# Performance work log

Hardware: AMD Instinct MI355X
Metric: run time of the kernel (lower is better)

Reference implementation:

```python
import jax, jax.numpy as jnp
import numpy as np

B, S, D = 2, 2048, 1024
H, HKV, DK = 16, 4, 64          # n_heads, n_kv_heads, head dim
NREP = H // HKV                  # 4


def apply_rope(x):
    # Faithful to the original: positions run over x.shape[-2], which is the
    # HEAD axis (x is [B, S, H, DK]) due to how the torch module is written.
    d = x.shape[-1]
    h = x.shape[-2]
    inv_freq = 1.0 / (10000.0 ** (jnp.arange(0, d, 2, dtype=jnp.float32) / d))
    freqs = jnp.arange(h, dtype=jnp.float32)[:, None] * inv_freq[None, :]  # [H, DK/2]
    cos, sin = jnp.cos(freqs), jnp.sin(freqs)
    x1, x2 = x[..., 0::2], x[..., 1::2]
    # interleave back: stack on new last axis then flatten
    return jnp.stack([x1 * cos - x2 * sin, x1 * sin + x2 * cos], axis=-1).reshape(x.shape)


def setup_inputs() -> dict:
    key = jax.random.key(0)
    kx, kq, kk, kv, ko = jax.random.split(key, 5)
    std = 0.02
    x = jax.random.normal(kx, (B, S, D), jnp.float32)
    w_q = jax.random.normal(kq, (D, H * DK), jnp.float32) * std
    w_k = jax.random.normal(kk, (D, HKV * DK), jnp.float32) * std
    w_v = jax.random.normal(kv, (D, HKV * DK), jnp.float32) * std
    w_o = jax.random.normal(ko, (D, D), jnp.float32) * std
    # causal mask, broadcastable to [B, H, S, S]
    mask = jnp.tril(jnp.ones((S, S), bool))[None, None]  # [1,1,S,S]
    return {"x": x, "w_q": w_q, "w_k": w_k, "w_v": w_v, "w_o": w_o, "mask": mask}


def reference(x, w_q, w_k, w_v, w_o, mask):
    b, s, d = x.shape
    Q = (x @ w_q).reshape(b, s, H, DK)
    K = (x @ w_k).reshape(b, s, HKV, DK)
    V = (x @ w_v).reshape(b, s, HKV, DK)
    Q = apply_rope(Q)
    K = apply_rope(K)
    # [B,H,S,DK] with query heads grouped per kv head (matches repeat_interleave)
    Q = Q.transpose(0, 2, 1, 3).reshape(b, HKV, NREP, s, DK)
    K = K.transpose(0, 2, 1, 3)  # [B,HKV,S,DK]
    V = V.transpose(0, 2, 1, 3)
    scores = jnp.einsum('bgrqd,bgkd->bgrqk', Q, K) / np.float32(np.sqrt(DK))
    scores = scores.astype(jnp.float32)
    neg = jnp.finfo(jnp.float32).min
    scores = jnp.where(mask[:, :, None, :, :], scores, neg)  # [1,1,1,S,S] broadcast
    w = jax.nn.softmax(scores, axis=-1)
    ctx = jnp.einsum('bgrqk,bgkd->bgrqd', w, V)  # [B,HKV,NREP,S,DK]
    ctx = ctx.reshape(b, H, s, DK).transpose(0, 2, 1, 3).reshape(b, s, d)
    return ctx @ w_o
```

## Files before the change

### kernel.cpp

```cpp
#include <hip/hip_runtime.h>
#include <hip/hip_bf16.h>

#define S_LEN 2048
#define NBATCH 2
#define DMODEL 1024
#define NHEAD 16
#define NKV 4
#define HDIM 64

typedef __attribute__((ext_vector_type(4))) float f32x4;
typedef __attribute__((ext_vector_type(8))) short s16x8;

#define QSCALE 0.18033688011112042f

__device__ __forceinline__ unsigned short f32_bf16(float f) {
    unsigned int u = __float_as_uint(f);
    u += 0x7FFFu + ((u >> 16) & 1u);
    return (unsigned short)(u >> 16);
}

__global__ __launch_bounds__(256) void cvt_bf16_k(const float* __restrict__ in,
                                                  unsigned short* __restrict__ out, int n4) {
    int i = blockIdx.x * 256 + threadIdx.x;
    if (i < n4) {
        const float4 v = reinterpret_cast<const float4*>(in)[i];
        ushort4 r;
        r.x = f32_bf16(v.x); r.y = f32_bf16(v.y);
        r.z = f32_bf16(v.z); r.w = f32_bf16(v.w);
        reinterpret_cast<ushort4*>(out)[i] = r;
    }
}

__global__ __launch_bounds__(256) void cvtT_k(const float* __restrict__ in,
                                              unsigned short* __restrict__ out,
                                              int N, int n_off) {
    __shared__ float t[64][65];
    const int n0  = blockIdx.x * 64;
    const int k0  = blockIdx.y * 64;
    const int tid = threadIdx.x;
    const int r   = tid >> 4;
    const int c4  = (tid & 15) * 4;
    #pragma unroll
    for (int i = 0; i < 4; ++i) {
        const float4 v = *reinterpret_cast<const float4*>(
            in + (size_t)(k0 + i*16 + r) * N + n0 + c4);
        t[i*16 + r][c4+0] = v.x; t[i*16 + r][c4+1] = v.y;
        t[i*16 + r][c4+2] = v.z; t[i*16 + r][c4+3] = v.w;
    }
    __syncthreads();
    #pragma unroll
    for (int i = 0; i < 4; ++i) {
        const int n = i*16 + r;
        ushort4 o;
        o.x = f32_bf16(t[c4+0][n]); o.y = f32_bf16(t[c4+1][n]);
        o.z = f32_bf16(t[c4+2][n]); o.w = f32_bf16(t[c4+3][n]);
        *reinterpret_cast<ushort4*>(out + (size_t)(n_off + n0 + n) * 1024 + k0 + c4) = o;
    }
}

template<int EPI>
__global__ __launch_bounds__(256, 2) void gemm2_k(
    const unsigned short* __restrict__ A,
    const unsigned short* __restrict__ Bt,
    int N, int K,
    float* __restrict__ OutF,
    unsigned short* __restrict__ Qb,
    unsigned short* __restrict__ Kbuf,
    unsigned short* __restrict__ Vbuf)
{
    __shared__ unsigned short As[2][128 * 64];
    __shared__ unsigned short Bs[2][64 * 64];

    const int tid  = threadIdx.x;
    const int lane = tid & 63;
    const int l15  = lane & 15;
    const int l4   = lane >> 4;
    const int wave = tid >> 6;
    const int wm   = wave >> 1;
    const int wn   = wave & 1;
    const int bm   = blockIdx.y * 128;
    const int bn   = blockIdx.x * 64;

    f32x4 acc[4][2] = {};
    s16x8 ar[4], br[2];

    const int NT = K >> 6;

    #define GLOAD(k0)                                                              \
        {                                                                          \
            _Pragma("unroll")                                                      \
            for (int p = 0; p < 4; ++p) {                                          \
                const int c = p*256 + tid, r_ = c >> 3, s_ = c & 7;                \
                ar[p] = *reinterpret_cast<const s16x8*>(                           \
                    A + (size_t)(bm + r_) * K + (k0) + s_*8);                      \
            }                                                                      \
            _Pragma("unroll")                                                      \
            for (int p = 0; p < 2; ++p) {                                          \
                const int c = p*256 + tid, r_ = c >> 3, s_ = c & 7;                \
                br[p] = *reinterpret_cast<const s16x8*>(                           \
                    Bt + (size_t)(bn + r_) * K + (k0) + s_*8);                     \
            }                                                                      \
        }
    #define LWRITE(buf)                                                            \
        {                                                                          \
            _Pragma("unroll")                                                      \
            for (int p = 0; p < 4; ++p) {                                          \
                const int c = p*256 + tid, r_ = c >> 3, s_ = c & 7;                \
                *reinterpret_cast<s16x8*>(                                         \
                    &As[buf][r_*64 + ((s_ ^ (r_ & 7)) * 8)]) = ar[p];              \
            }                                                                      \
            _Pragma("unroll")                                                      \
            for (int p = 0; p < 2; ++p) {                                          \
                const int c = p*256 + tid, r_ = c >> 3, s_ = c & 7;                \
                *reinterpret_cast<s16x8*>(                                         \
                    &Bs[buf][r_*64 + ((s_ ^ (r_ & 7)) * 8)]) = br[p];              \
            }                                                                      \
        }

    GLOAD(0); LWRITE(0); __syncthreads();

    for (int kt = 0; kt < NT; ++kt) {
        const int cur = kt & 1;
        if (kt + 1 < NT) GLOAD((kt + 1) << 6);
        #pragma unroll
        for (int ks = 0; ks < 2; ++ks) {
            s16x8 af[4], bfv[2];
            #pragma unroll
            for (int mi = 0; mi < 4; ++mi) {
                const int r = wm*64 + mi*16 + l15;
                af[mi] = *reinterpret_cast<const s16x8*>(
                    &As[cur][r*64 + (((ks*4 + l4) ^ (r & 7)) * 8)]);
            }
            #pragma unroll
            for (int nj = 0; nj < 2; ++nj) {
                const int r = wn*32 + nj*16 + l15;
                bfv[nj] = *reinterpret_cast<const s16x8*>(
                    &Bs[cur][r*64 + (((ks*4 + l4) ^ (r & 7)) * 8)]);
            }
            #pragma unroll
            for (int mi = 0; mi < 4; ++mi)
                #pragma unroll
                for (int nj = 0; nj < 2; ++nj)
                    acc[mi][nj] = __builtin_amdgcn_mfma_f32_16x16x32_bf16(
                        af[mi], bfv[nj], acc[mi][nj], 0, 0, 0);
        }
        if (kt + 1 < NT) LWRITE(cur ^ 1);
        __syncthreads();
    }
    #undef GLOAD
    #undef LWRITE

    #pragma unroll
    for (int mi = 0; mi < 4; ++mi) {
        #pragma unroll
        for (int nj = 0; nj < 2; ++nj) {
            #pragma unroll
            for (int v = 0; v < 4; ++v) {
                const int gr = bm + wm*64 + mi*16 + l4*4 + v;
                const int gc = bn + wn*32 + nj*16 + l15;
                float val = acc[mi][nj][v];
                if (EPI == 0) {
                    OutF[(size_t)gr * N + gc] = val;
                } else {
                    const int b  = gr >> 11;
                    const int sr = gr & (S_LEN - 1);
                    const int dk = gc & 63;
                    if (bn < 1024) {
                        const float partner = __shfl_xor(val, 1, 64);
                        const int   jp  = dk >> 1;
                        const float inv = __expf((float)jp * (-2.0f / 64.0f) * 9.210340371976184f);
                        const int   hh  = gc >> 6;
                        float sn, cs;
                        __sincosf((float)hh * inv, &sn, &cs);
                        val = ((gc & 1) == 0) ? (val * cs - partner * sn)
                                              : (partner * sn + val * cs);
                        val *= QSCALE;
                        Qb[(((size_t)b * NHEAD + hh) * S_LEN + sr) * HDIM + dk] = f32_bf16(val);
                    } else if (bn < 1280) {
                        const float partner = __shfl_xor(val, 1, 64);
                        const int   jp  = dk >> 1;
                        const float inv = __expf((float)jp * (-2.0f / 64.0f) * 9.210340371976184f);
                        const int   hh  = (gc - 1024) >> 6;
                        float sn, cs;
                        __sincosf((float)hh * inv, &sn, &cs);
                        val = ((gc & 1) == 0) ? (val * cs - partner * sn)
                                              : (partner * sn + val * cs);
                        Kbuf[(((size_t)b * NKV + hh) * S_LEN + sr) * HDIM + dk] = f32_bf16(val);
                    } else {
                        const int hh = (gc - 1280) >> 6;
                        Vbuf[(((size_t)b * NKV + hh) * HDIM + dk) * S_LEN + sr] = f32_bf16(val);
                    }
                }
            }
        }
    }
}


__device__ __forceinline__ void stage_load(
    const unsigned short* __restrict__ Kp,
    const unsigned short* __restrict__ Vp,
    int kv0, int tid, s16x8& kr, s16x8& vr)
{
    const int r = tid >> 3, col = (tid & 7) * 8;
    kr = *reinterpret_cast<const s16x8*>(Kp + (size_t)(kv0 + r) * HDIM + col);
    vr = *reinterpret_cast<const s16x8*>(Vp + (size_t)r * S_LEN + kv0 + col);
}

__device__ __forceinline__ void stage_write(
    unsigned short (*Ksb)[72], unsigned short (*Vsb)[72],
    int tid, const s16x8& kr, const s16x8& vr)
{
    const int r = tid >> 3, col = (tid & 7) * 8;
    *reinterpret_cast<s16x8*>(&Ksb[r][col]) = kr;
    *reinterpret_cast<s16x8*>(&Vsb[r][col]) = vr;
}

template<bool MASK>
__device__ __forceinline__ void attn_compute(
    int l15, int l4, int wloc,
    const unsigned short (*Ksb)[72], const unsigned short (*Vsb)[72],
    const s16x8 qf[2], f32x4 o[4], float& m, float& lsum,
    unsigned short (*Plds)[72])
{
    f32x4 s[4] = {};
    __builtin_amdgcn_s_setprio(1);
    #pragma unroll
    for (int c = 0; c < 4; ++c)
        #pragma unroll
        for (int ks = 0; ks < 2; ++ks) {
            const s16x8 kf = *reinterpret_cast<const s16x8*>(&Ksb[c*16 + l15][ks*32 + l4*8]);
            s[c] = __builtin_amdgcn_mfma_f32_16x16x32_bf16(kf, qf[ks], s[c], 0, 0, 0);
        }
    __builtin_amdgcn_s_setprio(0);

    if (MASK) {
        const int qloc = wloc + l15;
        #pragma unroll
        for (int c = 0; c < 4; ++c)
            #pragma unroll
            for (int v = 0; v < 4; ++v) {
                const int kvloc = c*16 + l4*4 + v;
                s[c][v] = (kvloc <= qloc) ? s[c][v] : -1e30f;
            }
    }

    float mx = -1e30f;
    #pragma unroll
    for (int c = 0; c < 4; ++c)
        #pragma unroll
        for (int v = 0; v < 4; ++v) mx = fmaxf(mx, s[c][v]);
    mx = fmaxf(mx, __shfl_xor(mx, 16, 64));
    mx = fmaxf(mx, __shfl_xor(mx, 32, 64));
    const float mnew  = fmaxf(m, mx);
    const float scale = __builtin_amdgcn_exp2f(m - mnew);
    float psum = 0.0f;
    #pragma unroll
    for (int c = 0; c < 4; ++c)
        #pragma unroll
        for (int v = 0; v < 4; ++v) {
            const float p = __builtin_amdgcn_exp2f(s[c][v] - mnew);
            s[c][v] = p;
            psum += p;
        }
    lsum = lsum * scale + psum;
    m = mnew;
    #pragma unroll
    for (int dkc = 0; dkc < 4; ++dkc) o[dkc] *= scale;

    #pragma unroll
    for (int c = 0; c < 4; ++c) {
        uint2 w;
        w.x = (unsigned int)f32_bf16(s[c][0]) | ((unsigned int)f32_bf16(s[c][1]) << 16);
        w.y = (unsigned int)f32_bf16(s[c][2]) | ((unsigned int)f32_bf16(s[c][3]) << 16);
        *reinterpret_cast<uint2*>(&Plds[l15][c*16 + l4*4]) = w;
    }
    s16x8 pb[2];
    #pragma unroll
    for (int ks = 0; ks < 2; ++ks)
        pb[ks] = *reinterpret_cast<const s16x8*>(&Plds[l15][ks*32 + l4*8]);

    __builtin_amdgcn_s_setprio(1);
    #pragma unroll
    for (int dkc = 0; dkc < 4; ++dkc)
        #pragma unroll
        for (int ks = 0; ks < 2; ++ks) {
            const s16x8 vf = *reinterpret_cast<const s16x8*>(&Vsb[dkc*16 + l15][ks*32 + l4*8]);
            o[dkc] = __builtin_amdgcn_mfma_f32_16x16x32_bf16(vf, pb[ks], o[dkc], 0, 0, 0);
        }
    __builtin_amdgcn_s_setprio(0);
}

__global__ __launch_bounds__(512, 2) void attn_k(
    const unsigned short* __restrict__ Q,
    const unsigned short* __restrict__ Kb,
    const unsigned short* __restrict__ Vt,
    unsigned short* __restrict__ Ctx)
{
    __shared__ unsigned short Ks[2][64][72];
    __shared__ unsigned short Vs[2][64][72];
    __shared__ unsigned short Plds[8][16][72];

    const int tid  = threadIdx.x;
    const int lane = tid & 63;
    const int l15  = lane & 15;
    const int l4   = lane >> 4;
    const int wave = tid >> 6;

    const int L  = blockIdx.x;
    const int h  = L & 15;
    const int b  = (L >> 4) & 1;
    const int p  = (L >> 5) & 7;
    const int qt = (L < 256) ? (15 - p) : p;
    const int qb0 = qt * 128;

    const int g   = h >> 2;

    const unsigned short* Qp = Q  + ((size_t)b * NHEAD + h) * S_LEN * HDIM;
    const unsigned short* Kp = Kb + ((size_t)b * NKV  + g) * S_LEN * HDIM;
    const unsigned short* Vp = Vt + ((size_t)b * NKV  + g) * HDIM * S_LEN;

    const int qb = qb0 + wave * 16;
    const int dt = qb >> 6;
    const int NT = qt * 2 + 2;

    s16x8 qf[2];
    #pragma unroll
    for (int ks = 0; ks < 2; ++ks)
        qf[ks] = *reinterpret_cast<const s16x8*>(Qp + (size_t)(qb + l15) * HDIM + ks*32 + l4*8);

    f32x4 o[4] = {};
    float m = -1e30f, lsum = 0.0f;

    {
        s16x8 kr, vr;
        stage_load(Kp, Vp, 0, tid, kr, vr);
        stage_write(Ks[0], Vs[0], tid, kr, vr);
        __syncthreads();
    }

    for (int t = 0; t < NT; ++t) {
        const int cur = t & 1;
        s16x8 kr, vr;
        const bool more = (t + 1 < NT);
        if (more) stage_load(Kp, Vp, (t + 1) * 64, tid, kr, vr);
        if (t < dt)
            attn_compute<false>(l15, l4, wave*16 - t*64 + qb0, Ks[cur], Vs[cur], qf, o, m, lsum, Plds[wave]);
        else if (t == dt)
            attn_compute<true >(l15, l4, wave*16 - t*64 + qb0, Ks[cur], Vs[cur], qf, o, m, lsum, Plds[wave]);
        if (more) stage_write(Ks[cur ^ 1], Vs[cur ^ 1], tid, kr, vr);
        __syncthreads();
    }

    lsum += __shfl_xor(lsum, 16, 64);
    lsum += __shfl_xor(lsum, 32, 64);
    const float inv = 1.0f / lsum;
    unsigned short* cp = Ctx + (((size_t)b * S_LEN + qb + l15) * NHEAD + h) * HDIM;
    #pragma unroll
    for (int dkc = 0; dkc < 4; ++dkc) {
        ushort4 r;
        r.x = f32_bf16(o[dkc][0] * inv);
        r.y = f32_bf16(o[dkc][1] * inv);
        r.z = f32_bf16(o[dkc][2] * inv);
        r.w = f32_bf16(o[dkc][3] * inv);
        *reinterpret_cast<ushort4*>(cp + dkc*16 + l4*4) = r;
    }
}

extern "C" void kernel_launch(void* const* d_in, const int* in_sizes, int n_in,
                              void* d_out, int out_size, void* d_ws, size_t ws_size,
                              hipStream_t stream) {
    const float* x  = (const float*)d_in[0];
    const float* wq = (const float*)d_in[1];
    const float* wk = (const float*)d_in[2];
    const float* wv = (const float*)d_in[3];
    const float* wo = (const float*)d_in[4];
    float* out = (float*)d_out;

    const int M  = NBATCH * S_LEN;
    const int nX = M * DMODEL;
    const int nQ = NBATCH * NHEAD * S_LEN * HDIM;
    const int nKV = NBATCH * NKV * S_LEN * HDIM;

    unsigned short* xb    = (unsigned short*)d_ws;
    unsigned short* Wqkvt = xb + nX;
    unsigned short* Wot   = Wqkvt + 1536 * 1024;
    unsigned short* Qb    = Wot + 1024 * 1024;
    unsigned short* Kb    = Qb + nQ;
    unsigned short* Vbuf  = Kb + nKV;
    unsigned short* Ctx   = xb;

    cvt_bf16_k<<<nX / 1024, 256, 0, stream>>>(x, xb, nX / 4);
    cvtT_k<<<dim3(16, 16), 256, 0, stream>>>(wq, Wqkvt, 1024, 0);
    cvtT_k<<<dim3( 4, 16), 256, 0, stream>>>(wk, Wqkvt,  256, 1024);
    cvtT_k<<<dim3( 4, 16), 256, 0, stream>>>(wv, Wqkvt,  256, 1280);
    cvtT_k<<<dim3(16, 16), 256, 0, stream>>>(wo, Wot,   1024, 0);

    gemm2_k<1><<<dim3(1536/64, M/128), 256, 0, stream>>>(
        xb, Wqkvt, 1536, DMODEL, nullptr, Qb, Kb, Vbuf);

    attn_k<<<dim3(512, 1, 1), 512, 0, stream>>>(Qb, Kb, Vbuf, Ctx);

    gemm2_k<0><<<dim3(DMODEL/64, M/128), 256, 0, stream>>>(
        Ctx, Wot, DMODEL, DMODEL, out, nullptr, nullptr, nullptr);
}
```

Baseline: 113.1 us.

## Enlarge GEMM tiles to 128x128, remap blocks per XCD, lazy softmax rescale

```diff
diff --git a/kernel.cpp b/kernel.cpp
--- a/kernel.cpp
+++ b/kernel.cpp
@@ -59,17 +59,17 @@
 }
 
 template<int EPI>
-__global__ __launch_bounds__(256, 2) void gemm2_k(
+__global__ __launch_bounds__(256, 2) void gemm3_k(
     const unsigned short* __restrict__ A,
     const unsigned short* __restrict__ Bt,
-    int N, int K,
+    int N, int K, int nbx,
     float* __restrict__ OutF,
     unsigned short* __restrict__ Qb,
     unsigned short* __restrict__ Kbuf,
     unsigned short* __restrict__ Vbuf)
 {
     __shared__ unsigned short As[2][128 * 64];
-    __shared__ unsigned short Bs[2][64 * 64];
+    __shared__ unsigned short Bs[2][128 * 64];
 
     const int tid  = threadIdx.x;
     const int lane = tid & 63;
@@ -78,11 +78,17 @@
     const int wave = tid >> 6;
     const int wm   = wave >> 1;
     const int wn   = wave & 1;
-    const int bm   = blockIdx.y * 128;
-    const int bn   = blockIdx.x * 64;
-
-    f32x4 acc[4][2] = {};
-    s16x8 ar[4], br[2];
+
+    const int nwg = gridDim.x;
+    const int cpx = nwg >> 3;
+    const int wg  = (blockIdx.x & 7) * cpx + (blockIdx.x >> 3);
+    const int bx  = wg % nbx;
+    const int by  = wg / nbx;
+    const int bm  = by * 128;
+    const int bn  = bx * 128;
+
+    f32x4 acc[4][4] = {};
+    s16x8 ar[4], br[4];
 
     const int NT = K >> 6;
 
@@ -90,30 +96,21 @@
         {                                                                          \
             _Pragma("unroll")                                                      \
             for (int p = 0; p < 4; ++p) {                                          \
-                const int c = p*256 + tid, r_ = c >> 3, s_ = c & 7;                \
+                const int c = p*256 + tid, r_ = c >> 3;                            \
+                const int nc = (c & 7) ^ (r_ & 7);                                 \
                 ar[p] = *reinterpret_cast<const s16x8*>(                           \
-                    A + (size_t)(bm + r_) * K + (k0) + s_*8);                      \
-            }                                                                      \
-            _Pragma("unroll")                                                      \
-            for (int p = 0; p < 2; ++p) {                                          \
-                const int c = p*256 + tid, r_ = c >> 3, s_ = c & 7;                \
+                    A + (size_t)(bm + r_) * K + (k0) + nc*8);                      \
                 br[p] = *reinterpret_cast<const s16x8*>(                           \
-                    Bt + (size_t)(bn + r_) * K + (k0) + s_*8);                     \
+                    Bt + (size_t)(bn + r_) * K + (k0) + nc*8);                     \
             }                                                                      \
         }
     #define LWRITE(buf)                                                            \
         {                                                                          \
             _Pragma("unroll")                                                      \
             for (int p = 0; p < 4; ++p) {                                          \
-                const int c = p*256 + tid, r_ = c >> 3, s_ = c & 7;                \
-                *reinterpret_cast<s16x8*>(                                         \
-                    &As[buf][r_*64 + ((s_ ^ (r_ & 7)) * 8)]) = ar[p];              \
-            }                                                                      \
-            _Pragma("unroll")                                                      \
-            for (int p = 0; p < 2; ++p) {                                          \
-                const int c = p*256 + tid, r_ = c >> 3, s_ = c & 7;                \
-                *reinterpret_cast<s16x8*>(                                         \
-                    &Bs[buf][r_*64 + ((s_ ^ (r_ & 7)) * 8)]) = br[p];              \
+                const int c = p*256 + tid;                                         \
+                *reinterpret_cast<s16x8*>(&As[buf][c*8]) = ar[p];                  \
+                *reinterpret_cast<s16x8*>(&Bs[buf][c*8]) = br[p];                  \
             }                                                                      \
         }
 
@@ -124,23 +121,23 @@
         if (kt + 1 < NT) GLOAD((kt + 1) << 6);
         #pragma unroll
         for (int ks = 0; ks < 2; ++ks) {
-            s16x8 af[4], bfv[2];
+            s16x8 af[4], bfv[4];
             #pragma unroll
             for (int mi = 0; mi < 4; ++mi) {
                 const int r = wm*64 + mi*16 + l15;
                 af[mi] = *reinterpret_cast<const s16x8*>(
-                    &As[cur][r*64 + (((ks*4 + l4) ^ (r & 7)) * 8)]);
+                    &As[cur][r*64 + (((ks*4 + l4) ^ (l15 & 7)) * 8)]);
             }
             #pragma unroll
-            for (int nj = 0; nj < 2; ++nj) {
-                const int r = wn*32 + nj*16 + l15;
+            for (int nj = 0; nj < 4; ++nj) {
+                const int r = wn*64 + nj*16 + l15;
                 bfv[nj] = *reinterpret_cast<const s16x8*>(
-                    &Bs[cur][r*64 + (((ks*4 + l4) ^ (r & 7)) * 8)]);
+                    &Bs[cur][r*64 + (((ks*4 + l4) ^ (l15 & 7)) * 8)]);
             }
             #pragma unroll
             for (int mi = 0; mi < 4; ++mi)
                 #pragma unroll
-                for (int nj = 0; nj < 2; ++nj)
+                for (int nj = 0; nj < 4; ++nj)
                     acc[mi][nj] = __builtin_amdgcn_mfma_f32_16x16x32_bf16(
                         af[mi], bfv[nj], acc[mi][nj], 0, 0, 0);
         }
@@ -153,11 +150,11 @@
     #pragma unroll
     for (int mi = 0; mi < 4; ++mi) {
         #pragma unroll
-        for (int nj = 0; nj < 2; ++nj) {
+        for (int nj = 0; nj < 4; ++nj) {
             #pragma unroll
             for (int v = 0; v < 4; ++v) {
                 const int gr = bm + wm*64 + mi*16 + l4*4 + v;
-                const int gc = bn + wn*32 + nj*16 + l15;
+                const int gc = bn + wn*64 + nj*16 + l15;
                 float val = acc[mi][nj][v];
                 if (EPI == 0) {
                     OutF[(size_t)gr * N + gc] = val;
@@ -252,21 +249,24 @@
         for (int v = 0; v < 4; ++v) mx = fmaxf(mx, s[c][v]);
     mx = fmaxf(mx, __shfl_xor(mx, 16, 64));
     mx = fmaxf(mx, __shfl_xor(mx, 32, 64));
-    const float mnew  = fmaxf(m, mx);
-    const float scale = __builtin_amdgcn_exp2f(m - mnew);
+    if (!__all(mx <= m + 8.0f)) {
+        const float mnew  = fmaxf(m, mx);
+        const float scale = __builtin_amdgcn_exp2f(m - mnew);
+        lsum *= scale;
+        #pragma unroll
+        for (int dkc = 0; dkc < 4; ++dkc) o[dkc] *= scale;
+        m = mnew;
+    }
     float psum = 0.0f;
     #pragma unroll
     for (int c = 0; c < 4; ++c)
         #pragma unroll
         for (int v = 0; v < 4; ++v) {
-            const float p = __builtin_amdgcn_exp2f(s[c][v] - mnew);
+            const float p = __builtin_amdgcn_exp2f(s[c][v] - m);
             s[c][v] = p;
             psum += p;
         }
-    lsum = lsum * scale + psum;
-    m = mnew;
-    #pragma unroll
-    for (int dkc = 0; dkc < 4; ++dkc) o[dkc] *= scale;
+    lsum += psum;
 
     #pragma unroll
     for (int c = 0; c < 4; ++c) {
@@ -396,11 +396,11 @@
     cvtT_k<<<dim3( 4, 16), 256, 0, stream>>>(wv, Wqkvt,  256, 1280);
     cvtT_k<<<dim3(16, 16), 256, 0, stream>>>(wo, Wot,   1024, 0);
 
-    gemm2_k<1><<<dim3(1536/64, M/128), 256, 0, stream>>>(
-        xb, Wqkvt, 1536, DMODEL, nullptr, Qb, Kb, Vbuf);
+    gemm3_k<1><<<dim3(384), 256, 0, stream>>>(
+        xb, Wqkvt, 1536, DMODEL, 12, nullptr, Qb, Kb, Vbuf);
 
     attn_k<<<dim3(512, 1, 1), 512, 0, stream>>>(Qb, Kb, Vbuf, Ctx);
 
-    gemm2_k<0><<<dim3(DMODEL/64, M/128), 256, 0, stream>>>(
-        Ctx, Wot, DMODEL, DMODEL, out, nullptr, nullptr, nullptr);
-}
+    gemm3_k<0><<<dim3(256), 256, 0, stream>>>(
+        Ctx, Wot, DMODEL, DMODEL, 8, out, nullptr, nullptr, nullptr);
+}
```

Measured after the change: 114.0 us. No clear change (+0.8%).

## Prefetch K/V two tiles ahead and skip softmax rescale when max is stable

Applied to the files above, without the earlier changes.

```diff
diff --git a/kernel.cpp b/kernel.cpp
--- a/kernel.cpp
+++ b/kernel.cpp
@@ -252,21 +252,24 @@
         for (int v = 0; v < 4; ++v) mx = fmaxf(mx, s[c][v]);
     mx = fmaxf(mx, __shfl_xor(mx, 16, 64));
     mx = fmaxf(mx, __shfl_xor(mx, 32, 64));
-    const float mnew  = fmaxf(m, mx);
-    const float scale = __builtin_amdgcn_exp2f(m - mnew);
+    if (!__all(mx <= m + 8.0f)) {
+        const float mnew  = fmaxf(m, mx);
+        const float scale = __builtin_amdgcn_exp2f(m - mnew);
+        lsum *= scale;
+        #pragma unroll
+        for (int dkc = 0; dkc < 4; ++dkc) o[dkc] *= scale;
+        m = mnew;
+    }
     float psum = 0.0f;
     #pragma unroll
     for (int c = 0; c < 4; ++c)
         #pragma unroll
         for (int v = 0; v < 4; ++v) {
-            const float p = __builtin_amdgcn_exp2f(s[c][v] - mnew);
+            const float p = __builtin_amdgcn_exp2f(s[c][v] - m);
             s[c][v] = p;
             psum += p;
         }
-    lsum = lsum * scale + psum;
-    m = mnew;
-    #pragma unroll
-    for (int dkc = 0; dkc < 4; ++dkc) o[dkc] *= scale;
+    lsum += psum;
 
     #pragma unroll
     for (int c = 0; c < 4; ++c) {
@@ -297,8 +300,8 @@
     const unsigned short* __restrict__ Vt,
     unsigned short* __restrict__ Ctx)
 {
-    __shared__ unsigned short Ks[2][64][72];
-    __shared__ unsigned short Vs[2][64][72];
+    __shared__ unsigned short Ks[3][64][72];
+    __shared__ unsigned short Vs[3][64][72];
     __shared__ unsigned short Plds[8][16][72];
 
     const int tid  = threadIdx.x;
@@ -332,23 +335,28 @@
     f32x4 o[4] = {};
     float m = -1e30f, lsum = 0.0f;
 
-    {
-        s16x8 kr, vr;
-        stage_load(Kp, Vp, 0, tid, kr, vr);
-        stage_write(Ks[0], Vs[0], tid, kr, vr);
-        __syncthreads();
-    }
+    s16x8 kr0, vr0, kr1, vr1;
+    stage_load(Kp, Vp, 0, tid, kr0, vr0);
+    stage_write(Ks[0], Vs[0], tid, kr0, vr0);
+    if (NT > 1) stage_load(Kp, Vp, 64, tid, kr1, vr1);
+    __syncthreads();
 
     for (int t = 0; t < NT; ++t) {
-        const int cur = t & 1;
-        s16x8 kr, vr;
-        const bool more = (t + 1 < NT);
-        if (more) stage_load(Kp, Vp, (t + 1) * 64, tid, kr, vr);
+        const int cur = t % 3;
+        const int nxt = (t + 1) % 3;
+        const bool even = (t & 1) == 0;
+        if (t + 2 < NT) {
+            if (even) stage_load(Kp, Vp, (t + 2) * 64, tid, kr0, vr0);
+            else      stage_load(Kp, Vp, (t + 2) * 64, tid, kr1, vr1);
+        }
         if (t < dt)
             attn_compute<false>(l15, l4, wave*16 - t*64 + qb0, Ks[cur], Vs[cur], qf, o, m, lsum, Plds[wave]);
         else if (t == dt)
             attn_compute<true >(l15, l4, wave*16 - t*64 + qb0, Ks[cur], Vs[cur], qf, o, m, lsum, Plds[wave]);
-        if (more) stage_write(Ks[cur ^ 1], Vs[cur ^ 1], tid, kr, vr);
+        if (t + 1 < NT) {
+            if (even) stage_write(Ks[nxt], Vs[nxt], tid, kr1, vr1);
+            else      stage_write(Ks[nxt], Vs[nxt], tid, kr0, vr0);
+        }
         __syncthreads();
     }
 
```

New measurement: 114.9 us. No clear change (+1.7%).

## Stage GEMM tiles via direct global-to-LDS loads and lazily rescale softmax

Applied to the files above, without the earlier changes.

```diff
diff --git a/kernel.cpp b/kernel.cpp
--- a/kernel.cpp
+++ b/kernel.cpp
@@ -58,8 +58,11 @@
     }
 }
 
+using gas_u32 = const unsigned int __attribute__((address_space(1))) *;
+using las_u32 = unsigned int __attribute__((address_space(3))) *;
+
 template<int EPI>
-__global__ __launch_bounds__(256, 2) void gemm2_k(
+__global__ __launch_bounds__(256, 3) void gemm2_k(
     const unsigned short* __restrict__ A,
     const unsigned short* __restrict__ Bt,
     int N, int K,
@@ -82,46 +85,34 @@
     const int bn   = blockIdx.x * 64;
 
     f32x4 acc[4][2] = {};
-    s16x8 ar[4], br[2];
 
     const int NT = K >> 6;
 
-    #define GLOAD(k0)                                                              \
+    #define GSTAGE(buf, k0)                                                        \
         {                                                                          \
             _Pragma("unroll")                                                      \
             for (int p = 0; p < 4; ++p) {                                          \
-                const int c = p*256 + tid, r_ = c >> 3, s_ = c & 7;                \
-                ar[p] = *reinterpret_cast<const s16x8*>(                           \
-                    A + (size_t)(bm + r_) * K + (k0) + s_*8);                      \
+                const int c = p*256 + tid, r_ = c >> 3;                            \
+                const int nc = (c & 7) ^ (r_ & 7);                                 \
+                __builtin_amdgcn_global_load_lds(                                  \
+                    (gas_u32)(A + (size_t)(bm + r_) * K + (k0) + nc*8),            \
+                    (las_u32)(&As[buf][c*8]), 16, 0, 0);                           \
             }                                                                      \
             _Pragma("unroll")                                                      \
             for (int p = 0; p < 2; ++p) {                                          \
-                const int c = p*256 + tid, r_ = c >> 3, s_ = c & 7;                \
-                br[p] = *reinterpret_cast<const s16x8*>(                           \
-                    Bt + (size_t)(bn + r_) * K + (k0) + s_*8);                     \
+                const int c = p*256 + tid, r_ = c >> 3;                            \
+                const int nc = (c & 7) ^ (r_ & 7);                                 \
+                __builtin_amdgcn_global_load_lds(                                  \
+                    (gas_u32)(Bt + (size_t)(bn + r_) * K + (k0) + nc*8),           \
+                    (las_u32)(&Bs[buf][c*8]), 16, 0, 0);                           \
             }                                                                      \
         }
-    #define LWRITE(buf)                                                            \
-        {                                                                          \
-            _Pragma("unroll")                                                      \
-            for (int p = 0; p < 4; ++p) {                                          \
-                const int c = p*256 + tid, r_ = c >> 3, s_ = c & 7;                \
-                *reinterpret_cast<s16x8*>(                                         \
-                    &As[buf][r_*64 + ((s_ ^ (r_ & 7)) * 8)]) = ar[p];              \
-            }                                                                      \
-            _Pragma("unroll")                                                      \
-            for (int p = 0; p < 2; ++p) {                                          \
-                const int c = p*256 + tid, r_ = c >> 3, s_ = c & 7;                \
-                *reinterpret_cast<s16x8*>(                                         \
-                    &Bs[buf][r_*64 + ((s_ ^ (r_ & 7)) * 8)]) = br[p];              \
-            }                                                                      \
-        }
-
-    GLOAD(0); LWRITE(0); __syncthreads();
+
+    GSTAGE(0, 0); __syncthreads();
 
     for (int kt = 0; kt < NT; ++kt) {
         const int cur = kt & 1;
-        if (kt + 1 < NT) GLOAD((kt + 1) << 6);
+        if (kt + 1 < NT) GSTAGE(cur ^ 1, (kt + 1) << 6);
         #pragma unroll
         for (int ks = 0; ks < 2; ++ks) {
             s16x8 af[4], bfv[2];
@@ -144,11 +135,9 @@
                     acc[mi][nj] = __builtin_amdgcn_mfma_f32_16x16x32_bf16(
                         af[mi], bfv[nj], acc[mi][nj], 0, 0, 0);
         }
-        if (kt + 1 < NT) LWRITE(cur ^ 1);
         __syncthreads();
     }
-    #undef GLOAD
-    #undef LWRITE
+    #undef GSTAGE
 
     #pragma unroll
     for (int mi = 0; mi < 4; ++mi) {
@@ -252,21 +241,24 @@
         for (int v = 0; v < 4; ++v) mx = fmaxf(mx, s[c][v]);
     mx = fmaxf(mx, __shfl_xor(mx, 16, 64));
     mx = fmaxf(mx, __shfl_xor(mx, 32, 64));
-    const float mnew  = fmaxf(m, mx);
-    const float scale = __builtin_amdgcn_exp2f(m - mnew);
+    if (!__all(mx <= m + 8.0f)) {
+        const float mnew  = fmaxf(m, mx);
+        const float scale = __builtin_amdgcn_exp2f(m - mnew);
+        lsum *= scale;
+        #pragma unroll
+        for (int dkc = 0; dkc < 4; ++dkc) o[dkc] *= scale;
+        m = mnew;
+    }
     float psum = 0.0f;
     #pragma unroll
     for (int c = 0; c < 4; ++c)
         #pragma unroll
         for (int v = 0; v < 4; ++v) {
-            const float p = __builtin_amdgcn_exp2f(s[c][v] - mnew);
+            const float p = __builtin_amdgcn_exp2f(s[c][v] - m);
             s[c][v] = p;
             psum += p;
         }
-    lsum = lsum * scale + psum;
-    m = mnew;
-    #pragma unroll
-    for (int dkc = 0; dkc < 4; ++dkc) o[dkc] *= scale;
+    lsum += psum;
 
     #pragma unroll
     for (int c = 0; c < 4; ++c) {
```

Result: faster. 104.8 us (-7.3%).
